# Performance work log

Measured on AMD Instinct MI355X. Metric: run time of the kernel, lower is better.

## Reference

```python
import jax, jax.numpy as jnp
import numpy as np

N_NODES = 50000
N_EDGES = 800000
IN_CH = 128
HID = 256
OUT_CH = 10
N_GRAPHS = 64


def setup_inputs() -> dict:
    key = jax.random.key(0)
    ks = jax.random.split(key, 16)
    s = 0.02
    inp = {
        "x": jax.random.normal(ks[0], (N_NODES, IN_CH), dtype=jnp.float32),
        "edge_index": jax.random.randint(ks[1], (2, N_EDGES), 0, N_NODES, dtype=jnp.int64),
        "batch": jnp.sort(jax.random.randint(ks[2], (N_NODES,), 0, N_GRAPHS, dtype=jnp.int64)),
        # SAGEConv params: out = lin_l(mean_agg) + lin_r(x_root); lin_l has bias, lin_r does not (PyG default)
        "W1l": jax.random.normal(ks[3], (HID, IN_CH), dtype=jnp.float32) * s,
        "b1": jnp.zeros((HID,), jnp.float32),
        "W1r": jax.random.normal(ks[4], (HID, IN_CH), dtype=jnp.float32) * s,
        "W2l": jax.random.normal(ks[5], (HID, HID), dtype=jnp.float32) * s,
        "b2": jnp.zeros((HID,), jnp.float32),
        "W2r": jax.random.normal(ks[6], (HID, HID), dtype=jnp.float32) * s,
        "W3l": jax.random.normal(ks[7], (HID, HID), dtype=jnp.float32) * s,
        "b3": jnp.zeros((HID,), jnp.float32),
        "W3r": jax.random.normal(ks[8], (HID, HID), dtype=jnp.float32) * s,
        "lin1_W": jax.random.normal(ks[9], (HID // 2, HID), dtype=jnp.float32) * s,
        "lin1_b": jnp.zeros((HID // 2,), jnp.float32),
        "lin2_W": jax.random.normal(ks[10], (OUT_CH, HID // 2), dtype=jnp.float32) * s,
        "lin2_b": jnp.zeros((OUT_CH,), jnp.float32),
    }
    return inp


def _sage_conv(x, src, dst, Wl, bl, Wr):
    # mean-aggregate neighbor features at destination nodes
    msg_sum = jax.ops.segment_sum(x[src], dst, num_segments=N_NODES)  # [N, d]
    deg = jax.ops.segment_sum(jnp.ones((src.shape[0],), x.dtype), dst, num_segments=N_NODES)
    agg = msg_sum / jnp.maximum(deg, 1.0)[:, None]
    return agg @ Wl.T + bl + x @ Wr.T


def reference(x, edge_index, batch, W1l, b1, W1r, W2l, b2, W2r, W3l, b3, W3r,
              lin1_W, lin1_b, lin2_W, lin2_b):
    src, dst = edge_index[0], edge_index[1]
    h = jax.nn.relu(_sage_conv(x, src, dst, W1l, b1, W1r))
    h = jax.nn.relu(_sage_conv(h, src, dst, W2l, b2, W2r))
    h = jax.nn.relu(_sage_conv(h, src, dst, W3l, b3, W3r))
    # global_mean_pool over batch vector
    pooled_sum = jax.ops.segment_sum(h, batch, num_segments=N_GRAPHS)  # [G, HID]
    counts = jax.ops.segment_sum(jnp.ones((h.shape[0],), h.dtype), batch, num_segments=N_GRAPHS)
    g = pooled_sum / jnp.maximum(counts, 1.0)[:, None]
    g = jax.nn.relu(g @ lin1_W.T + lin1_b)
    # dropout is identity in eval mode
    return g @ lin2_W.T + lin2_b
```

## Files before the change

kernel.cpp:

```cpp
#include <hip/hip_runtime.h>
#include <hip/hip_bf16.h>


#define HID 256
typedef unsigned short ushort_t;
typedef __bf16 bf16x8 __attribute__((ext_vector_type(8)));
typedef float  f32x4  __attribute__((ext_vector_type(4)));
typedef float  f32x2  __attribute__((ext_vector_type(2)));

__device__ __forceinline__ unsigned short f2bf(float f) {
    unsigned int u = __float_as_uint(f);
    unsigned int r = (u + 0x7fffu + ((u >> 16) & 1u)) >> 16;
    return (unsigned short)r;
}
__device__ __forceinline__ float bflo(unsigned int u) { return __uint_as_float(u << 16); }
__device__ __forceinline__ float bfhi(unsigned int u) { return __uint_as_float(u & 0xffff0000u); }
__device__ __forceinline__ unsigned int packbf(float a, float b) {
    return (unsigned int)f2bf(a) | ((unsigned int)f2bf(b) << 16);
}
__device__ __forceinline__ void gld16(const void* g, void* l) {
    __builtin_amdgcn_global_load_lds(
        (const __attribute__((address_space(1))) unsigned int*)g,
        (__attribute__((address_space(3))) unsigned int*)l, 16, 0, 0);
}
__device__ __forceinline__ void fma8(float* a, float w, const uint4 v) {
    a[0] = fmaf(w, bflo(v.x), a[0]); a[1] = fmaf(w, bfhi(v.x), a[1]);
    a[2] = fmaf(w, bflo(v.y), a[2]); a[3] = fmaf(w, bfhi(v.y), a[3]);
    a[4] = fmaf(w, bflo(v.z), a[4]); a[5] = fmaf(w, bfhi(v.z), a[5]);
    a[6] = fmaf(w, bflo(v.w), a[6]); a[7] = fmaf(w, bfhi(v.w), a[7]);
}
__device__ __forceinline__ void fma8_f8(float* a, float w, const uint2 v) {
    const f32x2 c01 = __builtin_amdgcn_cvt_pk_f32_fp8(v.x, false);
    const f32x2 c23 = __builtin_amdgcn_cvt_pk_f32_fp8(v.x, true);
    const f32x2 c45 = __builtin_amdgcn_cvt_pk_f32_fp8(v.y, false);
    const f32x2 c67 = __builtin_amdgcn_cvt_pk_f32_fp8(v.y, true);
    a[0] = fmaf(w, c01.x, a[0]); a[1] = fmaf(w, c01.y, a[1]);
    a[2] = fmaf(w, c23.x, a[2]); a[3] = fmaf(w, c23.y, a[3]);
    a[4] = fmaf(w, c45.x, a[4]); a[5] = fmaf(w, c45.y, a[5]);
    a[6] = fmaf(w, c67.x, a[6]); a[7] = fmaf(w, c67.y, a[7]);
}
__device__ __forceinline__ int4 load4idx(const int* __restrict__ csr, int pbase, int e1m1) {
    int4 r;
    r.x = csr[min(pbase + 0, e1m1)];
    r.y = csr[min(pbase + 1, e1m1)];
    r.z = csr[min(pbase + 2, e1m1)];
    r.w = csr[min(pbase + 3, e1m1)];
    return r;
}

#define NBUCK 256
#define NPB_BUCK 196
#define BCAP 4096

__global__ __launch_bounds__(256)
void cvt_kernel(const float* __restrict__ x, ushort_t* __restrict__ xb, int nx4,
                const float* __restrict__ W1l, const float* __restrict__ W1r,
                const float* __restrict__ W2l, const float* __restrict__ W2r,
                const float* __restrict__ W3l, const float* __restrict__ W3r,
                ushort_t* __restrict__ wdst, int s1, int s2,
                int* __restrict__ bcursor, float* __restrict__ pooled) {
    const int t = blockIdx.x * 256 + threadIdx.x;
    if (t < NBUCK) bcursor[t] = 0;
    if (t < 64 * 256 / 4) *(float4*)(pooled + t * 4) = make_float4(0.f, 0.f, 0.f, 0.f);
    if (t < nx4) {
        const int i = t * 4;
        const float4 v = *(const float4*)(x + i);
        *(uint2*)(xb + i) = make_uint2(packbf(v.x, v.y), packbf(v.z, v.w));
        return;
    }
    int off = t - nx4;
    const int total = 2 * s1 + 4 * s2;
    if (off >= total) return;
    const int i = off;
    const float* src;
    if (off < s1) src = W1l;
    else if ((off -= s1) < s1) src = W1r;
    else if ((off -= s1) < s2) src = W2l;
    else if ((off -= s2) < s2) src = W2r;
    else if ((off -= s2) < s2) src = W3l;
    else { off -= s2; src = W3r; }
    wdst[i] = f2bf(src[off]);
}

__global__ __launch_bounds__(256)
void binA_kernel(const int* __restrict__ src, const int* __restrict__ dst,
                 int* __restrict__ bcursor, unsigned int* __restrict__ staging, int E) {
    __shared__ int hist[NBUCK];
    __shared__ int wbase[NBUCK];
    const int tid = threadIdx.x;
    hist[tid] = 0;
    __syncthreads();
    const int i0 = blockIdx.x * 2048;
    int d8[8], s8[8], b8[8];
    #pragma unroll
    for (int j = 0; j < 8; ++j) {
        const int i = i0 + j * 256 + tid;
        if (i < E) {
            d8[j] = dst[i];
            s8[j] = src[i];
            b8[j] = d8[j] / NPB_BUCK;
            atomicAdd(&hist[b8[j]], 1);
        } else b8[j] = -1;
    }
    __syncthreads();
    {
        const int b = tid;
        const int cnt = hist[b];
        int wb = 0;
        if (cnt > 0) wb = atomicAdd(&bcursor[b], cnt);
        wbase[b] = b * BCAP + wb;
        hist[b] = 0;
    }
    __syncthreads();
    #pragma unroll
    for (int j = 0; j < 8; ++j) {
        if (b8[j] >= 0) {
            const int pos = wbase[b8[j]] + atomicAdd(&hist[b8[j]], 1);
            if (pos < (b8[j] + 1) * BCAP)
                staging[pos] = ((unsigned int)(d8[j] - b8[j] * NPB_BUCK) << 16) | (unsigned int)s8[j];
        }
    }
}

__global__ __launch_bounds__(256)
void binB_kernel(const unsigned int* __restrict__ staging, const int* __restrict__ bcursor,
                 int* __restrict__ csr, int* __restrict__ offsets, int nn, int E) {
    __shared__ unsigned int sedge[BCAP];
    __shared__ int cnt[NBUCK];
    __shared__ int bsum[4];
    __shared__ int wt[4];
    const int b = blockIdx.x, tid = threadIdx.x;
    const int lane = tid & 63, wid = tid >> 6;

    int part = (tid < b) ? bcursor[tid] : 0;
    #pragma unroll
    for (int d = 1; d < 64; d <<= 1) part += __shfl_xor(part, d, 64);
    if (lane == 0) bsum[wid] = part;
    const int mycnt = min(bcursor[b], BCAP);
    __syncthreads();
    const int base = bsum[0] + bsum[1] + bsum[2] + bsum[3];

    for (int i = tid; i < mycnt; i += 256) sedge[i] = staging[b * BCAP + i];
    cnt[tid] = 0;
    __syncthreads();
    for (int i = tid; i < mycnt; i += 256) atomicAdd(&cnt[sedge[i] >> 16], 1);
    __syncthreads();

    const int v = cnt[tid];
    int incl = v;
    #pragma unroll
    for (int d = 1; d < 64; d <<= 1) {
        int t = __shfl_up(incl, d, 64);
        if (lane >= d) incl += t;
    }
    if (lane == 63) wt[wid] = incl;
    __syncthreads();
    int wb = 0;
    #pragma unroll
    for (int w = 0; w < 4; ++w) { int t = wt[w]; if (w < wid) wb += t; }
    const int excl = wb + incl - v;

    const int node = b * NPB_BUCK + tid;
    if (tid < NPB_BUCK && node < nn) offsets[node] = base + excl;
    if (b == NBUCK - 1 && tid == 0) offsets[nn] = E;
    __syncthreads();
    cnt[tid] = excl;
    __syncthreads();

    for (int i = tid; i < mycnt; i += 256) {
        const unsigned int e = sedge[i];
        const int p = atomicAdd(&cnt[e >> 16], 1);
        csr[base + p] = (int)(e & 0xFFFFu);
    }
}

template <int C>
__global__ __launch_bounds__(256)
void agg_kernel(const ushort_t* __restrict__ h, const int* __restrict__ offsets,
                const int* __restrict__ csr, ushort_t* __restrict__ out, int nn) {
    constexpr int CL = C / 8;
    constexpr int EW = 64 / CL;
    constexpr int RPE = 4 * EW;
    const int node = (blockIdx.x * 256 + threadIdx.x) >> 6;
    if (node >= nn) return;
    const int lane = threadIdx.x & 63;
    const int cl = lane & (CL - 1);
    const int eo = lane / CL;
    const int e0 = offsets[node], e1 = offsets[node + 1];
    const int deg = e1 - e0;
    const int rounds = (deg + RPE - 1) / RPE;
    const int e1m1 = max(e1 - 1, 0);
    float a[8] = {0.f, 0.f, 0.f, 0.f, 0.f, 0.f, 0.f, 0.f};
    int pb = e0 + eo * 4;
    if (rounds > 0) {
        int4 idx = load4idx(csr, pb, e1m1);
        for (int r2 = 0; r2 < rounds; ++r2) {
            const int4 cur = idx;
            const int pcur = pb;
            pb += RPE;
            if (r2 + 1 < rounds) idx = load4idx(csr, pb, e1m1);
            const uint4 v0 = *(const uint4*)(h + (size_t)cur.x * C + cl * 8);
            const uint4 v1 = *(const uint4*)(h + (size_t)cur.y * C + cl * 8);
            const uint4 v2 = *(const uint4*)(h + (size_t)cur.z * C + cl * 8);
            const uint4 v3 = *(const uint4*)(h + (size_t)cur.w * C + cl * 8);
            fma8(a, (pcur + 0 < e1) ? 1.f : 0.f, v0);
            fma8(a, (pcur + 1 < e1) ? 1.f : 0.f, v1);
            fma8(a, (pcur + 2 < e1) ? 1.f : 0.f, v2);
            fma8(a, (pcur + 3 < e1) ? 1.f : 0.f, v3);
        }
    }
    #pragma unroll
    for (int d = CL; d < 64; d <<= 1)
        #pragma unroll
        for (int r = 0; r < 8; ++r) a[r] += __shfl_xor(a[r], d, 64);
    if (eo == 0) {
        const float inv = 1.0f / fmaxf((float)deg, 1.0f);
        uint4 o;
        o.x = packbf(a[0] * inv, a[1] * inv);
        o.y = packbf(a[2] * inv, a[3] * inv);
        o.z = packbf(a[4] * inv, a[5] * inv);
        o.w = packbf(a[6] * inv, a[7] * inv);
        *(uint4*)(out + (size_t)node * C + cl * 8) = o;
    }
}

__global__ __launch_bounds__(256)
void agg8_kernel(const unsigned char* __restrict__ h8, const int* __restrict__ offsets,
                 const int* __restrict__ csr, ushort_t* __restrict__ out, int nn) {
    const int node = (blockIdx.x * 256 + threadIdx.x) >> 6;
    if (node >= nn) return;
    const int lane = threadIdx.x & 63;
    const int cl = lane & 31;
    const int eo = lane >> 5;
    const int e0 = offsets[node], e1 = offsets[node + 1];
    const int deg = e1 - e0;
    const int rounds = (deg + 7) / 8;
    const int e1m1 = max(e1 - 1, 0);
    float a[8] = {0.f, 0.f, 0.f, 0.f, 0.f, 0.f, 0.f, 0.f};
    int pb = e0 + eo * 4;
    if (rounds > 0) {
        int4 idx = load4idx(csr, pb, e1m1);
        for (int r2 = 0; r2 < rounds; ++r2) {
            const int4 cur = idx;
            const int pcur = pb;
            pb += 8;
            if (r2 + 1 < rounds) idx = load4idx(csr, pb, e1m1);
            const uint2 v0 = *(const uint2*)(h8 + (size_t)cur.x * 256 + cl * 8);
            const uint2 v1 = *(const uint2*)(h8 + (size_t)cur.y * 256 + cl * 8);
            const uint2 v2 = *(const uint2*)(h8 + (size_t)cur.z * 256 + cl * 8);
            const uint2 v3 = *(const uint2*)(h8 + (size_t)cur.w * 256 + cl * 8);
            fma8_f8(a, (pcur + 0 < e1) ? 1.f : 0.f, v0);
            fma8_f8(a, (pcur + 1 < e1) ? 1.f : 0.f, v1);
            fma8_f8(a, (pcur + 2 < e1) ? 1.f : 0.f, v2);
            fma8_f8(a, (pcur + 3 < e1) ? 1.f : 0.f, v3);
        }
    }
    #pragma unroll
    for (int r = 0; r < 8; ++r) a[r] += __shfl_xor(a[r], 32, 64);
    if (eo == 0) {
        const float inv = 1.0f / fmaxf((float)deg, 1.0f);
        uint4 o;
        o.x = packbf(a[0] * inv, a[1] * inv);
        o.y = packbf(a[2] * inv, a[3] * inv);
        o.z = packbf(a[4] * inv, a[5] * inv);
        o.w = packbf(a[6] * inv, a[7] * inv);
        *(uint4*)(out + (size_t)node * 256 + cl * 8) = o;
    }
}

template <int K, bool W8>
__global__ __launch_bounds__(256, 2)
void gemm2_mfma(const ushort_t* __restrict__ A1, const ushort_t* __restrict__ A2,
                const ushort_t* __restrict__ W1, const ushort_t* __restrict__ W2,
                const float* __restrict__ bias, ushort_t* __restrict__ Cout,
                unsigned char* __restrict__ H8, int M) {
    __shared__ ushort_t As[2 * 128 * 64];
    __shared__ ushort_t Bs[2 * 128 * 64];
    const int tid = threadIdx.x;
    const int row0 = blockIdx.x * 128, col0 = blockIdx.y * 128;
    const int wave = tid >> 6, lane = tid & 63;
    const int wm = (wave & 1) * 64, wn = (wave >> 1) * 64;
    const int l15 = lane & 15, quad = lane >> 4;
    constexpr int NCH = K / 128;

    f32x4 acc[4][4] = {};

    #pragma unroll
    for (int phase = 0; phase < 2; ++phase) {
        const ushort_t* __restrict__ A = phase ? A2 : A1;
        const ushort_t* __restrict__ W = phase ? W2 : W1;
        for (int kc = 0; kc < NCH; ++kc) {
            const int kt = kc * 128;
            __syncthreads();
            #pragma unroll
            for (int p = 0; p < 8; ++p) {
                const int slot = p * 256 + tid;
                const int g = slot >> 10;
                const int r = (slot >> 3) & 127;
                const int c = slot & 7;
                const int cg = c ^ (r & 7);
                int ar = row0 + r; if (ar >= M) ar = M - 1;
                gld16(A + (size_t)ar * K + kt + g * 64 + cg * 8, &As[slot * 8]);
            }
            #pragma unroll
            for (int p = 0; p < 8; ++p) {
                const int slot = p * 256 + tid;
                const int g = slot >> 10;
                const int r = (slot >> 3) & 127;
                const int c = slot & 7;
                const int cg = c ^ (r & 7);
                gld16(W + (size_t)(col0 + r) * K + kt + g * 64 + cg * 8, &Bs[slot * 8]);
            }
            __syncthreads();
            #pragma unroll
            for (int g = 0; g < 2; ++g) {
                #pragma unroll
                for (int ks = 0; ks < 2; ++ks) {
                    const int kq = ks * 4 + quad;
                    bf16x8 af[4], bfv[4];
                    #pragma unroll
                    for (int i = 0; i < 4; ++i) {
                        const int r = wm + i * 16 + l15;
                        const int cl = kq ^ (r & 7);
                        af[i] = *(const bf16x8*)&As[g * 8192 + r * 64 + cl * 8];
                    }
                    #pragma unroll
                    for (int j = 0; j < 4; ++j) {
                        const int r = wn + j * 16 + l15;
                        const int cl = kq ^ (r & 7);
                        bfv[j] = *(const bf16x8*)&Bs[g * 8192 + r * 64 + cl * 8];
                    }
                    #pragma unroll
                    for (int i = 0; i < 4; ++i)
                        #pragma unroll
                        for (int j = 0; j < 4; ++j)
                            acc[i][j] = __builtin_amdgcn_mfma_f32_16x16x32_bf16(
                                af[i], bfv[j], acc[i][j], 0, 0, 0);
                }
            }
        }
    }

    #pragma unroll
    for (int i = 0; i < 4; ++i) {
        const int mbase = row0 + wm + i * 16 + quad * 4;
        #pragma unroll
        for (int j = 0; j < 4; ++j) {
            const int n = col0 + wn + j * 16 + l15;
            const float b = bias[n];
            #pragma unroll
            for (int reg = 0; reg < 4; ++reg) {
                const int mr = mbase + reg;
                const float v = fmaxf(acc[i][j][reg] + b, 0.f);
                const float vp = __shfl_xor(v, 1, 64);
                if (!(l15 & 1) && mr < M)
                    *(unsigned int*)(Cout + (size_t)mr * 256 + n) = packbf(v, vp);
                if (W8) {
                    const int p2 = __builtin_amdgcn_cvt_pk_fp8_f32(v, vp, 0, false);
                    const int q2 = __shfl_xor(p2, 2, 64);
                    if ((l15 & 3) == 0 && mr < M)
                        *(unsigned int*)(H8 + (size_t)mr * 256 + n) =
                            ((unsigned int)p2 & 0xFFFFu) | ((unsigned int)q2 << 16);
                }
            }
        }
    }
}

__global__ __launch_bounds__(256)
void pool_partial_kernel(const ushort_t* __restrict__ h, const int* __restrict__ batch,
                         float* __restrict__ pooled, int nn) {
    const int n0 = blockIdx.x * 64;
    if (n0 >= nn) return;
    const int n1 = min(n0 + 64, nn);
    const int tid = threadIdx.x;
    const int cl = tid & 31, rg = tid >> 5;
    const int g0 = batch[n0];
    const int g1 = batch[n1 - 1];
    float a0[8] = {0.f, 0.f, 0.f, 0.f, 0.f, 0.f, 0.f, 0.f};
    float a1[8] = {0.f, 0.f, 0.f, 0.f, 0.f, 0.f, 0.f, 0.f};
    for (int n = n0 + rg; n < n1; n += 8) {
        const uint4 v = *(const uint4*)(h + (size_t)n * 256 + cl * 8);
        const float w1 = (batch[n] != g0) ? 1.f : 0.f;
        fma8(a0, 1.f - w1, v);
        fma8(a1, w1, v);
    }
    __shared__ float red[8][512];
    #pragma unroll
    for (int r = 0; r < 8; ++r) {
        red[rg][cl * 8 + r] = a0[r];
        red[rg][256 + cl * 8 + r] = a1[r];
    }
    __syncthreads();
    float s0 = 0.f, s1 = 0.f;
    #pragma unroll
    for (int r = 0; r < 8; ++r) { s0 += red[r][tid]; s1 += red[r][256 + tid]; }
    atomicAdd(&pooled[g0 * 256 + tid], s0);
    if (g1 != g0) atomicAdd(&pooled[g1 * 256 + tid], s1);
}

__global__ __launch_bounds__(256)
void mlp_kernel(const float* __restrict__ pooled, const int* __restrict__ batch, int nn,
                const float* __restrict__ lin1W, const float* __restrict__ lin1b,
                const float* __restrict__ lin2W, const float* __restrict__ lin2b,
                float* __restrict__ out) {
    const int g = blockIdx.x;
    const int tid = threadIdx.x;
    int lo = 0, hi = nn;
    while (lo < hi) { int mid = (lo + hi) >> 1; if (batch[mid] < g) lo = mid + 1; else hi = mid; }
    const int s = lo;
    hi = nn;
    while (lo < hi) { int mid = (lo + hi) >> 1; if (batch[mid] < g + 1) lo = mid + 1; else hi = mid; }
    const int e = lo;
    __shared__ float meanv[256];
    __shared__ float g1v[128];
    meanv[tid] = pooled[g * 256 + tid] / fmaxf((float)(e - s), 1.0f);
    __syncthreads();
    if (tid < 128) {
        float acc = lin1b[tid];
        #pragma unroll 4
        for (int k = 0; k < 256; k += 4) {
            const float4 w = *(const float4*)(lin1W + tid * 256 + k);
            acc += meanv[k] * w.x + meanv[k + 1] * w.y + meanv[k + 2] * w.z + meanv[k + 3] * w.w;
        }
        g1v[tid] = fmaxf(acc, 0.f);
    }
    __syncthreads();
    if (tid < 10) {
        float o = lin2b[tid];
        #pragma unroll 4
        for (int k = 0; k < 128; k += 4) {
            const float4 w = *(const float4*)(lin2W + tid * 128 + k);
            o += g1v[k] * w.x + g1v[k + 1] * w.y + g1v[k + 2] * w.z + g1v[k + 3] * w.w;
        }
        out[g * 10 + tid] = o;
    }
}

extern "C" void kernel_launch(void* const* d_in, const int* in_sizes, int n_in,
                              void* d_out, int out_size, void* d_ws, size_t ws_size,
                              hipStream_t stream) {
    const float* x     = (const float*)d_in[0];
    const int*   eidx  = (const int*)d_in[1];
    const int*   batch = (const int*)d_in[2];
    const float* W1l = (const float*)d_in[3];
    const float* b1  = (const float*)d_in[4];
    const float* W1r = (const float*)d_in[5];
    const float* W2l = (const float*)d_in[6];
    const float* b2  = (const float*)d_in[7];
    const float* W2r = (const float*)d_in[8];
    const float* W3l = (const float*)d_in[9];
    const float* b3  = (const float*)d_in[10];
    const float* W3r = (const float*)d_in[11];
    const float* lin1W = (const float*)d_in[12];
    const float* lin1b = (const float*)d_in[13];
    const float* lin2W = (const float*)d_in[14];
    const float* lin2b = (const float*)d_in[15];
    float* out = (float*)d_out;

    const int E  = in_sizes[1] / 2;
    const int NN = in_sizes[2];
    const int IN = 128;
    const int* src = eidx;
    const int* dst = eidx + E;

    char* ws = (char*)d_ws;
    size_t off = 0;
    auto alloc = [&](size_t bytes) { void* p = ws + off; off += (bytes + 255) / 256 * 256; return p; };
    ushort_t* xb  = (ushort_t*)alloc((size_t)NN * IN * 2);
    ushort_t* agg = (ushort_t*)alloc((size_t)NN * HID * 2);
    ushort_t* hA  = (ushort_t*)alloc((size_t)NN * HID * 2);
    ushort_t* hB  = (ushort_t*)alloc((size_t)NN * HID * 2);
    unsigned char* h8 = (unsigned char*)alloc((size_t)NN * HID);
    const int s1 = HID * IN, s2 = HID * HID;
    ushort_t* wb  = (ushort_t*)alloc((size_t)(2 * s1 + 4 * s2) * 2);
    int* offsets   = (int*)alloc((size_t)(NN + 1) * 4);
    int* csr       = (int*)alloc((size_t)E * 4);
    unsigned int* staging = (unsigned int*)alloc((size_t)NBUCK * BCAP * 4);
    int* bcursor   = (int*)alloc(NBUCK * 4);
    float* pooled  = (float*)alloc(64 * 256 * 4);
    (void)ws_size; (void)n_in; (void)out_size;

    const ushort_t* W1lb = wb;
    const ushort_t* W1rb = wb + s1;
    const ushort_t* W2lb = wb + 2 * s1;
    const ushort_t* W2rb = wb + 2 * s1 + s2;
    const ushort_t* W3lb = wb + 2 * s1 + 2 * s2;
    const ushort_t* W3rb = wb + 2 * s1 + 3 * s2;

    const int TB = 256;
    const int mgrid = (NN + 127) / 128;

    const int nx4 = NN * IN / 4;
    const int wtotal = 2 * s1 + 4 * s2;
    cvt_kernel<<<(nx4 + wtotal + TB - 1) / TB, TB, 0, stream>>>(
        x, xb, nx4, W1l, W1r, W2l, W2r, W3l, W3r, wb, s1, s2, bcursor, pooled);

    binA_kernel<<<(E + 2047) / 2048, TB, 0, stream>>>(src, dst, bcursor, staging, E);
    binB_kernel<<<NBUCK, TB, 0, stream>>>(staging, bcursor, csr, offsets, NN, E);

    agg_kernel<128><<<(NN + 3) / 4, TB, 0, stream>>>(xb, offsets, csr, agg, NN);
    gemm2_mfma<128, true><<<dim3(mgrid, 2), TB, 0, stream>>>(agg, xb, W1lb, W1rb, b1, hA, h8, NN);
    agg8_kernel<<<(NN + 3) / 4, TB, 0, stream>>>(h8, offsets, csr, agg, NN);
    gemm2_mfma<256, true><<<dim3(mgrid, 2), TB, 0, stream>>>(agg, hA, W2lb, W2rb, b2, hB, h8, NN);
    agg8_kernel<<<(NN + 3) / 4, TB, 0, stream>>>(h8, offsets, csr, agg, NN);
    gemm2_mfma<256, false><<<dim3(mgrid, 2), TB, 0, stream>>>(agg, hB, W3lb, W3rb, b3, hA, nullptr, NN);

    pool_partial_kernel<<<(NN + 63) / 64, TB, 0, stream>>>(hA, batch, pooled, NN);
    mlp_kernel<<<64, TB, 0, stream>>>(pooled, batch, NN, lin1W, lin1b, lin2W, lin2b, out);
}
```

Measured before the change: 338.8 us.

## Load GEMM operands directly from global into registers, dropping LDS staging

```diff
diff --git a/kernel.cpp b/kernel.cpp
--- a/kernel.cpp
+++ b/kernel.cpp
@@ -17,11 +17,6 @@
 __device__ __forceinline__ float bfhi(unsigned int u) { return __uint_as_float(u & 0xffff0000u); }
 __device__ __forceinline__ unsigned int packbf(float a, float b) {
     return (unsigned int)f2bf(a) | ((unsigned int)f2bf(b) << 16);
-}
-__device__ __forceinline__ void gld16(const void* g, void* l) {
-    __builtin_amdgcn_global_load_lds(
-        (const __attribute__((address_space(1))) unsigned int*)g,
-        (__attribute__((address_space(3))) unsigned int*)l, 16, 0, 0);
 }
 __device__ __forceinline__ void fma8(float* a, float w, const uint4 v) {
     a[0] = fmaf(w, bflo(v.x), a[0]); a[1] = fmaf(w, bfhi(v.x), a[1]);
@@ -269,76 +264,51 @@
 }
 
 template <int K, bool W8>
-__global__ __launch_bounds__(256, 2)
+__global__ __launch_bounds__(256, 3)
 void gemm2_mfma(const ushort_t* __restrict__ A1, const ushort_t* __restrict__ A2,
                 const ushort_t* __restrict__ W1, const ushort_t* __restrict__ W2,
                 const float* __restrict__ bias, ushort_t* __restrict__ Cout,
                 unsigned char* __restrict__ H8, int M) {
-    __shared__ ushort_t As[2 * 128 * 64];
-    __shared__ ushort_t Bs[2 * 128 * 64];
     const int tid = threadIdx.x;
     const int row0 = blockIdx.x * 128, col0 = blockIdx.y * 128;
     const int wave = tid >> 6, lane = tid & 63;
     const int wm = (wave & 1) * 64, wn = (wave >> 1) * 64;
     const int l15 = lane & 15, quad = lane >> 4;
-    constexpr int NCH = K / 128;
+
+    size_t aoff[4], boff[4];
+    #pragma unroll
+    for (int i = 0; i < 4; ++i) {
+        aoff[i] = (size_t)min(row0 + wm + i * 16 + l15, M - 1) * K + quad * 8;
+        boff[i] = (size_t)(col0 + wn + i * 16 + l15) * K + quad * 8;
+    }
+
+    constexpr int CPP = K / 32;
+    constexpr int T = 2 * CPP;
 
     f32x4 acc[4][4] = {};
-
-    #pragma unroll
-    for (int phase = 0; phase < 2; ++phase) {
-        const ushort_t* __restrict__ A = phase ? A2 : A1;
-        const ushort_t* __restrict__ W = phase ? W2 : W1;
-        for (int kc = 0; kc < NCH; ++kc) {
-            const int kt = kc * 128;
-            __syncthreads();
+    bf16x8 afb[2][4], bfb[2][4];
+
+    auto stage = [&](int t, int buf) {
+        const ushort_t* __restrict__ A = (t >= CPP) ? A2 : A1;
+        const ushort_t* __restrict__ W = (t >= CPP) ? W2 : W1;
+        const int kk = (t % CPP) * 32;
+        #pragma unroll
+        for (int i = 0; i < 4; ++i) afb[buf][i] = *(const bf16x8*)(A + aoff[i] + kk);
+        #pragma unroll
+        for (int j = 0; j < 4; ++j) bfb[buf][j] = *(const bf16x8*)(W + boff[j] + kk);
+    };
+
+    stage(0, 0);
+    #pragma unroll
+    for (int t = 0; t < T; ++t) {
+        const int cur = t & 1;
+        if (t + 1 < T) stage(t + 1, 1 - cur);
+        #pragma unroll
+        for (int i = 0; i < 4; ++i)
             #pragma unroll
-            for (int p = 0; p < 8; ++p) {
-                const int slot = p * 256 + tid;
-                const int g = slot >> 10;
-                const int r = (slot >> 3) & 127;
-                const int c = slot & 7;
-                const int cg = c ^ (r & 7);
-                int ar = row0 + r; if (ar >= M) ar = M - 1;
-                gld16(A + (size_t)ar * K + kt + g * 64 + cg * 8, &As[slot * 8]);
-            }
-            #pragma unroll
-            for (int p = 0; p < 8; ++p) {
-                const int slot = p * 256 + tid;
-                const int g = slot >> 10;
-                const int r = (slot >> 3) & 127;
-                const int c = slot & 7;
-                const int cg = c ^ (r & 7);
-                gld16(W + (size_t)(col0 + r) * K + kt + g * 64 + cg * 8, &Bs[slot * 8]);
-            }
-            __syncthreads();
-            #pragma unroll
-            for (int g = 0; g < 2; ++g) {
-                #pragma unroll
-                for (int ks = 0; ks < 2; ++ks) {
-                    const int kq = ks * 4 + quad;
-                    bf16x8 af[4], bfv[4];
-                    #pragma unroll
-                    for (int i = 0; i < 4; ++i) {
-                        const int r = wm + i * 16 + l15;
-                        const int cl = kq ^ (r & 7);
-                        af[i] = *(const bf16x8*)&As[g * 8192 + r * 64 + cl * 8];
-                    }
-                    #pragma unroll
-                    for (int j = 0; j < 4; ++j) {
-                        const int r = wn + j * 16 + l15;
-                        const int cl = kq ^ (r & 7);
-                        bfv[j] = *(const bf16x8*)&Bs[g * 8192 + r * 64 + cl * 8];
-                    }
-                    #pragma unroll
-                    for (int i = 0; i < 4; ++i)
-                        #pragma unroll
-                        for (int j = 0; j < 4; ++j)
-                            acc[i][j] = __builtin_amdgcn_mfma_f32_16x16x32_bf16(
-                                af[i], bfv[j], acc[i][j], 0, 0, 0);
-                }
-            }
-        }
+            for (int j = 0; j < 4; ++j)
+                acc[i][j] = __builtin_amdgcn_mfma_f32_16x16x32_bf16(
+                    afb[cur][i], bfb[cur][j], acc[i][j], 0, 0, 0);
     }
 
     #pragma unroll
```

After: 425.5 us. +25.6%, slower.

## Load GEMM weight fragments directly from global into registers with double buffering

Applied to the files above, without the earlier changes.

```diff
diff --git a/kernel.cpp b/kernel.cpp
--- a/kernel.cpp
+++ b/kernel.cpp
@@ -269,26 +269,41 @@
 }
 
 template <int K, bool W8>
-__global__ __launch_bounds__(256, 2)
+__global__ __launch_bounds__(256, 3)
 void gemm2_mfma(const ushort_t* __restrict__ A1, const ushort_t* __restrict__ A2,
                 const ushort_t* __restrict__ W1, const ushort_t* __restrict__ W2,
                 const float* __restrict__ bias, ushort_t* __restrict__ Cout,
                 unsigned char* __restrict__ H8, int M) {
     __shared__ ushort_t As[2 * 128 * 64];
-    __shared__ ushort_t Bs[2 * 128 * 64];
     const int tid = threadIdx.x;
     const int row0 = blockIdx.x * 128, col0 = blockIdx.y * 128;
     const int wave = tid >> 6, lane = tid & 63;
     const int wm = (wave & 1) * 64, wn = (wave >> 1) * 64;
     const int l15 = lane & 15, quad = lane >> 4;
     constexpr int NCH = K / 128;
+    constexpr int CPP = K / 32;
+    constexpr int TC = 2 * CPP;
+
+    size_t boff[4];
+    #pragma unroll
+    for (int j = 0; j < 4; ++j)
+        boff[j] = (size_t)(col0 + wn + j * 16 + l15) * K + quad * 8;
 
     f32x4 acc[4][4] = {};
-
+    bf16x8 bfb[2][4];
+
+    auto loadB = [&](int t, int buf) {
+        const ushort_t* __restrict__ W = (t >= CPP) ? W2 : W1;
+        const int kk = (t % CPP) * 32;
+        #pragma unroll
+        for (int j = 0; j < 4; ++j) bfb[buf][j] = *(const bf16x8*)(W + boff[j] + kk);
+    };
+
+    loadB(0, 0);
+    int t = 0;
     #pragma unroll
     for (int phase = 0; phase < 2; ++phase) {
         const ushort_t* __restrict__ A = phase ? A2 : A1;
-        const ushort_t* __restrict__ W = phase ? W2 : W1;
         for (int kc = 0; kc < NCH; ++kc) {
             const int kt = kc * 128;
             __syncthreads();
@@ -302,22 +317,15 @@
                 int ar = row0 + r; if (ar >= M) ar = M - 1;
                 gld16(A + (size_t)ar * K + kt + g * 64 + cg * 8, &As[slot * 8]);
             }
-            #pragma unroll
-            for (int p = 0; p < 8; ++p) {
-                const int slot = p * 256 + tid;
-                const int g = slot >> 10;
-                const int r = (slot >> 3) & 127;
-                const int c = slot & 7;
-                const int cg = c ^ (r & 7);
-                gld16(W + (size_t)(col0 + r) * K + kt + g * 64 + cg * 8, &Bs[slot * 8]);
-            }
             __syncthreads();
             #pragma unroll
             for (int g = 0; g < 2; ++g) {
                 #pragma unroll
                 for (int ks = 0; ks < 2; ++ks) {
+                    const int cur = t & 1;
+                    if (t + 1 < TC) loadB(t + 1, 1 - cur);
                     const int kq = ks * 4 + quad;
-                    bf16x8 af[4], bfv[4];
+                    bf16x8 af[4];
                     #pragma unroll
                     for (int i = 0; i < 4; ++i) {
                         const int r = wm + i * 16 + l15;
@@ -325,17 +333,12 @@
                         af[i] = *(const bf16x8*)&As[g * 8192 + r * 64 + cl * 8];
                     }
                     #pragma unroll
-                    for (int j = 0; j < 4; ++j) {
-                        const int r = wn + j * 16 + l15;
-                        const int cl = kq ^ (r & 7);
-                        bfv[j] = *(const bf16x8*)&Bs[g * 8192 + r * 64 + cl * 8];
-                    }
-                    #pragma unroll
                     for (int i = 0; i < 4; ++i)
                         #pragma unroll
                         for (int j = 0; j < 4; ++j)
                             acc[i][j] = __builtin_amdgcn_mfma_f32_16x16x32_bf16(
-                                af[i], bfv[j], acc[i][j], 0, 0, 0);
+                                af[i], bfb[cur][j], acc[i][j], 0, 0, 0);
+                    ++t;
                 }
             }
         }
```

Measured after the change: 363.1 us. +7.2%, slower.
